# Performance work log

Hardware: AMD Instinct MI355X
Metric: run time of the kernel (lower is better)

## Reference

```python
import jax, jax.numpy as jnp
import numpy as np

TOPK = 32  # init kwarg topk=32, method='softmax'


def setup_inputs() -> dict:
    key = jax.random.key(0)
    k1, k2 = jax.random.split(key)
    X1 = jax.random.normal(k1, (8192, 64), dtype=jnp.float32)
    X2 = jax.random.normal(k2, (8192, 64), dtype=jnp.float32)
    return {"X1": X1, "X2": X2}


def reference(X1, X2):
    # pairwise Euclidean distance via the matmul expansion (same math as torch.cdist p=2)
    sq = (
        jnp.sum(X1 * X1, axis=-1)[:, None]
        + jnp.sum(X2 * X2, axis=-1)[None, :]
        - 2.0 * (X1 @ X2.T)
    )  # [N1, N2]
    neg_dist = -jnp.sqrt(jnp.maximum(sq, 0.0))
    # top-k along dim=1, softmax over the k selected values
    val, idx = jax.lax.top_k(neg_dist, TOPK)          # [N1, K]
    score = jax.nn.softmax(val, axis=1)               # [N1, K]
    # scatter scores back into a dense zero matrix
    rows = jnp.arange(neg_dist.shape[0])[:, None]     # [N1, 1]
    out = jnp.zeros_like(neg_dist).at[rows, idx].set(score)
    return out, score
```

## Files before the change

kernel.cpp:

```cpp
#include <hip/hip_runtime.h>
#include <math.h>
#include <float.h>
#include <limits.h>

#define N 8192
#define D 64
#define TOPK 32
#define TILE 128
#define CAP 1024

__device__ __forceinline__ unsigned ford(float f) {
    unsigned u = __float_as_uint(f);
    return u ^ ((u & 0x80000000u) ? 0xFFFFFFFFu : 0x80000000u);
}
__device__ __forceinline__ float finv(unsigned u) {
    unsigned b = (u & 0x80000000u) ? (u ^ 0x80000000u) : ~u;
    return __uint_as_float(b);
}

__global__ __launch_bounds__(256) void norms_kernel(
    const float* __restrict__ X1, const float* __restrict__ X2,
    float* __restrict__ nrm)
{
    int id = blockIdx.x * blockDim.x + threadIdx.x;
    if (id >= 2 * N) return;
    const float* X = (id < N) ? X1 : X2;
    int r = (id < N) ? id : id - N;
    const float4* p = (const float4*)(X + (size_t)r * D);
    float s = 0.f;
#pragma unroll
    for (int q = 0; q < D / 4; ++q) {
        float4 v = p[q];
        s += v.x * v.x + v.y * v.y + v.z * v.z + v.w * v.w;
    }
    nrm[id] = s;
}

__global__ __launch_bounds__(256, 2) void dist_kernel(
    const float* __restrict__ X1, const float* __restrict__ X2,
    const float* __restrict__ nrm, float* __restrict__ out,
    float* __restrict__ tmax, int have_tmax)
{
    __shared__ float As[D * TILE];
    __shared__ float Bs[D * TILE];

    const int t = threadIdx.x;
    const int row0 = blockIdx.y * TILE;
    const int col0 = blockIdx.x * TILE;

#pragma unroll
    for (int p = 0; p < 8; ++p) {
        int lin = p * 256 + t;
        int r   = lin >> 4;
        int d4  = (lin & 15) << 2;
        int g   = (d4 >> 2) & 7;
        int cb  = r ^ (g << 3);
        float4 a = *(const float4*)(X1 + (size_t)(row0 + r) * D + d4);
        As[(d4 + 0) * TILE + cb] = a.x;
        As[(d4 + 1) * TILE + cb] = a.y;
        As[(d4 + 2) * TILE + cb] = a.z;
        As[(d4 + 3) * TILE + cb] = a.w;
        float4 b = *(const float4*)(X2 + (size_t)(col0 + r) * D + d4);
        Bs[(d4 + 0) * TILE + cb] = b.x;
        Bs[(d4 + 1) * TILE + cb] = b.y;
        Bs[(d4 + 2) * TILE + cb] = b.z;
        Bs[(d4 + 3) * TILE + cb] = b.w;
    }
    __syncthreads();

    const int tx = t & 15;
    const int ty = t >> 4;
    float acc[8][8] = {};

#pragma unroll 8
    for (int k = 0; k < D; ++k) {
        int gk  = (k >> 2) & 7;
        int ab  = k * TILE + ((ty ^ gk) << 3);
        int bb0 = k * TILE + ((4 * tx) ^ (gk << 3));
        float4 a0 = *(const float4*)&As[ab];
        float4 a1 = *(const float4*)&As[ab + 4];
        float4 b0 = *(const float4*)&Bs[bb0];
        float4 b1 = *(const float4*)&Bs[bb0 + 64];
        float av[8] = {a0.x, a0.y, a0.z, a0.w, a1.x, a1.y, a1.z, a1.w};
        float bv[8] = {b0.x, b0.y, b0.z, b0.w, b1.x, b1.y, b1.z, b1.w};
#pragma unroll
        for (int i = 0; i < 8; ++i)
#pragma unroll
            for (int j = 0; j < 8; ++j)
                acc[i][j] += av[i] * bv[j];
    }

    float na[8], nb[8];
#pragma unroll
    for (int i = 0; i < 8; ++i) na[i] = nrm[row0 + 8 * ty + i];
#pragma unroll
    for (int q = 0; q < 4; ++q) {
        nb[q]     = nrm[N + col0 + 4 * tx + q];
        nb[4 + q] = nrm[N + col0 + 64 + 4 * tx + q];
    }

    float rmax[8];
#pragma unroll
    for (int i = 0; i < 8; ++i) rmax[i] = -FLT_MAX;

#pragma unroll
    for (int i = 0; i < 8; ++i) {
        float* po = out + (size_t)(row0 + 8 * ty + i) * N + col0 + 4 * tx;
        float4 o0, o1;
        float* f0 = (float*)&o0;
        float* f1 = (float*)&o1;
#pragma unroll
        for (int q = 0; q < 4; ++q) {
            float s0 = na[i] + nb[q] - 2.0f * acc[i][q];
            f0[q] = -fmaxf(s0, 0.0f);
            float s1 = na[i] + nb[4 + q] - 2.0f * acc[i][4 + q];
            f1[q] = -fmaxf(s1, 0.0f);
            rmax[i] = fmaxf(rmax[i], fmaxf(f0[q], f1[q]));
        }
        *(float4*)po        = o0;
        *(float4*)(po + 64) = o1;
    }

    if (have_tmax) {
#pragma unroll
        for (int i = 0; i < 8; ++i) {
            float mv = rmax[i];
            mv = fmaxf(mv, __shfl_down(mv, 8, 16));
            mv = fmaxf(mv, __shfl_down(mv, 4, 16));
            mv = fmaxf(mv, __shfl_down(mv, 2, 16));
            mv = fmaxf(mv, __shfl_down(mv, 1, 16));
            if (tx == 0)
                tmax[(size_t)(row0 + 8 * ty + i) * 64 + blockIdx.x] = mv;
        }
    }
}

__global__ __launch_bounds__(256) void topk_kernel(
    float* __restrict__ out, float* __restrict__ score_out,
    const float* __restrict__ tmax, int have_tmax)
{
    __shared__ unsigned long long cand[4][CAP];
    __shared__ int scnt[4];

    const int t    = threadIdx.x;
    const int w    = t >> 6;
    const int lane = t & 63;
    const int r    = blockIdx.x * 4 + w;
    float* row = out + (size_t)r * N;
    const float4* row4 = (const float4*)row;

    float thr;
    float lm = -FLT_MAX;
    if (have_tmax) {
        float tm = tmax[(size_t)r * 64 + lane];
        unsigned km = ford(tm);
        int rk = 0;
#pragma unroll
        for (int l = 0; l < 64; ++l) {
            unsigned o = __shfl(km, l);
            rk += (o > km || (o == km && l < lane)) ? 1 : 0;
        }
        unsigned long long bm = __ballot(rk == 31);
        thr = __shfl(tm, __ffsll(bm) - 1);
    } else {
#pragma unroll 8
        for (int c = 0; c < 32; ++c) {
            float4 x = row4[c * 64 + lane];
            lm = fmaxf(lm, fmaxf(fmaxf(x.x, x.y), fmaxf(x.z, x.w)));
        }
        thr = lm;
        for (int off = 32; off > 0; off >>= 1)
            thr = fminf(thr, __shfl_xor(thr, off));
    }

    for (int attempt = 0; ; ++attempt) {
        if (lane == 0) scnt[w] = 0;
        __builtin_amdgcn_s_waitcnt(0xC07F);
        for (int c = 0; c < 32; ++c) {
            float4 x = row4[c * 64 + lane];
            float vs[4] = {x.x, x.y, x.z, x.w};
#pragma unroll
            for (int q = 0; q < 4; ++q) {
                float v = vs[q];
                lm = fmaxf(lm, v);
                if (v >= thr) {
                    int p = atomicAdd(&scnt[w], 1);
                    if (p < CAP) {
                        unsigned long long key =
                            ((unsigned long long)ford(v) << 32) |
                            (unsigned)(8191 - (4 * (c * 64 + lane) + q));
                        cand[w][p] = key;
                    }
                }
            }
        }
        __builtin_amdgcn_s_waitcnt(0xC07F);
        if (scnt[w] <= CAP || attempt == 1) break;
        unsigned kml = ford(lm);
        int rk2 = 0;
#pragma unroll
        for (int l = 0; l < 64; ++l) {
            unsigned o = __shfl(kml, l);
            rk2 += (o < kml || (o == kml && l < lane)) ? 1 : 0;
        }
        unsigned long long bm2 = __ballot(rk2 == 15);
        float t2 = __shfl(lm, __ffsll(bm2) - 1);
        thr = fmaxf(thr, t2);
    }
    const int n = min(scnt[w], CAP);

    unsigned long long mykey = 0ull;
    for (int it = 0; it < TOPK; ++it) {
        unsigned long long b = 0ull; int bp = 0;
        for (int q = lane; q < n; q += 64) {
            unsigned long long kk = cand[w][q];
            if (kk > b) { b = kk; bp = q; }
        }
        for (int off = 32; off > 0; off >>= 1) {
            unsigned long long ob = __shfl_down(b, off);
            int op = __shfl_down(bp, off);
            if (ob > b) { b = ob; bp = op; }
        }
        unsigned long long b0 = __shfl(b, 0);
        int bp0 = __shfl(bp, 0);
        if (lane == it) { mykey = b0; cand[w][bp0] = 0ull; }
    }

    float myv = 0.f; int myj = 0;
    if (lane < TOPK) {
        float sv = finv((unsigned)(mykey >> 32));
        myv = -sqrtf(-sv);
        myj = 8191 - (int)(mykey & 0xFFFFFFFFu);
    }
    float Mx = __shfl(myv, 0);
    float e = (lane < TOPK) ? expf(myv - Mx) : 0.f;
    float Z = e;
    for (int off = 32; off > 0; off >>= 1) Z += __shfl_xor(Z, off);
    float s = e / Z;
    if (lane < TOPK) score_out[(size_t)r * TOPK + lane] = s;

    const float4 zz = make_float4(0.f, 0.f, 0.f, 0.f);
#pragma unroll 8
    for (int c = 0; c < 32; ++c) ((float4*)row)[c * 64 + lane] = zz;
    __builtin_amdgcn_s_waitcnt(0x0F70);
    if (lane < TOPK) row[myj] = s;
}

extern "C" void kernel_launch(void* const* d_in, const int* in_sizes, int n_in,
                              void* d_out, int out_size, void* d_ws, size_t ws_size,
                              hipStream_t stream)
{
    const float* X1 = (const float*)d_in[0];
    const float* X2 = (const float*)d_in[1];
    float* out = (float*)d_out;
    float* nrm = (float*)d_ws;
    float* tmax = nrm + 2 * N;
    size_t need = (size_t)(2 * N + (size_t)N * 64) * sizeof(float);
    int have_tmax = (ws_size >= need) ? 1 : 0;

    norms_kernel<<<(2 * N + 255) / 256, 256, 0, stream>>>(X1, X2, nrm);

    dim3 grid(N / TILE, N / TILE);
    dist_kernel<<<grid, 256, 0, stream>>>(X1, X2, nrm, out, tmax, have_tmax);

    topk_kernel<<<N / 4, 256, 0, stream>>>(out, out + (size_t)N * N, tmax, have_tmax);
}
```

Measured before the change: 476.3 us.

## Recompute distances instead of storing them; gather candidates in fused zero-writing pass

```diff
diff --git a/kernel.cpp b/kernel.cpp
--- a/kernel.cpp
+++ b/kernel.cpp
@@ -8,6 +8,8 @@
 #define TOPK 32
 #define TILE 128
 #define CAP 1024
+#define CAPC 512
+#define NCHUNK 8
 
 __device__ __forceinline__ unsigned ford(float f) {
     unsigned u = __float_as_uint(f);
@@ -36,10 +38,9 @@
     nrm[id] = s;
 }
 
-__global__ __launch_bounds__(256, 2) void dist_kernel(
+__global__ __launch_bounds__(256, 2) void dist_tmax_kernel(
     const float* __restrict__ X1, const float* __restrict__ X2,
-    const float* __restrict__ nrm, float* __restrict__ out,
-    float* __restrict__ tmax, int have_tmax)
+    const float* __restrict__ nrm, float* __restrict__ tmax)
 {
     __shared__ float As[D * TILE];
     __shared__ float Bs[D * TILE];
@@ -99,6 +100,270 @@
         nb[4 + q] = nrm[N + col0 + 64 + 4 * tx + q];
     }
 
+#pragma unroll
+    for (int i = 0; i < 8; ++i) {
+        float mv = -FLT_MAX;
+#pragma unroll
+        for (int q = 0; q < 4; ++q) {
+            float s0 = na[i] + nb[q] - 2.0f * acc[i][q];
+            float v0 = -fmaxf(s0, 0.0f);
+            float s1 = na[i] + nb[4 + q] - 2.0f * acc[i][4 + q];
+            float v1 = -fmaxf(s1, 0.0f);
+            mv = fmaxf(mv, fmaxf(v0, v1));
+        }
+        mv = fmaxf(mv, __shfl_down(mv, 8, 16));
+        mv = fmaxf(mv, __shfl_down(mv, 4, 16));
+        mv = fmaxf(mv, __shfl_down(mv, 2, 16));
+        mv = fmaxf(mv, __shfl_down(mv, 1, 16));
+        if (tx == 0)
+            tmax[(size_t)(row0 + 8 * ty + i) * 64 + blockIdx.x] = mv;
+    }
+}
+
+__global__ __launch_bounds__(256) void thr_kernel(
+    const float* __restrict__ tmax, float* __restrict__ thr,
+    int* __restrict__ cnt)
+{
+    const int t = threadIdx.x;
+    const int w = t >> 6;
+    const int lane = t & 63;
+    const int r = blockIdx.x * 4 + w;
+
+    float tm = tmax[(size_t)r * 64 + lane];
+    unsigned km = ford(tm);
+    int rk = 0;
+#pragma unroll
+    for (int l = 0; l < 64; ++l) {
+        unsigned o = __shfl(km, l);
+        rk += (o > km || (o == km && l < lane)) ? 1 : 0;
+    }
+    unsigned long long bm = __ballot(rk == 31);
+    float tv = __shfl(tm, __ffsll(bm) - 1);
+    if (lane == 0) {
+        thr[r] = tv - 1e-3f;
+        cnt[r] = 0;
+    }
+}
+
+__global__ __launch_bounds__(256, 2) void cand_zero_kernel(
+    const float* __restrict__ X1, const float* __restrict__ X2,
+    const float* __restrict__ nrm, const float* __restrict__ thr,
+    float* __restrict__ out, unsigned long long* __restrict__ cand,
+    int* __restrict__ cnt)
+{
+    __shared__ float As[D * TILE];
+    __shared__ float Bs[D * TILE];
+
+    const int t = threadIdx.x;
+    const int row0 = blockIdx.y * TILE;
+    const int chunk0 = blockIdx.x * (N / NCHUNK);
+    const int tx = t & 15;
+    const int ty = t >> 4;
+
+#pragma unroll
+    for (int p = 0; p < 8; ++p) {
+        int lin = p * 256 + t;
+        int r   = lin >> 4;
+        int d4  = (lin & 15) << 2;
+        int g   = (d4 >> 2) & 7;
+        int cb  = r ^ (g << 3);
+        float4 a = *(const float4*)(X1 + (size_t)(row0 + r) * D + d4);
+        As[(d4 + 0) * TILE + cb] = a.x;
+        As[(d4 + 1) * TILE + cb] = a.y;
+        As[(d4 + 2) * TILE + cb] = a.z;
+        As[(d4 + 3) * TILE + cb] = a.w;
+    }
+
+    float na[8], thv[8];
+#pragma unroll
+    for (int i = 0; i < 8; ++i) {
+        na[i]  = nrm[row0 + 8 * ty + i];
+        thv[i] = thr[row0 + 8 * ty + i];
+    }
+    __syncthreads();
+
+    for (int ct = 0; ct < (N / NCHUNK) / TILE; ++ct) {
+        const int col0 = chunk0 + ct * TILE;
+        if (ct) __syncthreads();
+#pragma unroll
+        for (int p = 0; p < 8; ++p) {
+            int lin = p * 256 + t;
+            int r   = lin >> 4;
+            int d4  = (lin & 15) << 2;
+            int g   = (d4 >> 2) & 7;
+            int cb  = r ^ (g << 3);
+            float4 b = *(const float4*)(X2 + (size_t)(col0 + r) * D + d4);
+            Bs[(d4 + 0) * TILE + cb] = b.x;
+            Bs[(d4 + 1) * TILE + cb] = b.y;
+            Bs[(d4 + 2) * TILE + cb] = b.z;
+            Bs[(d4 + 3) * TILE + cb] = b.w;
+        }
+        __syncthreads();
+
+        float acc[8][8] = {};
+#pragma unroll 8
+        for (int k = 0; k < D; ++k) {
+            int gk  = (k >> 2) & 7;
+            int ab  = k * TILE + ((ty ^ gk) << 3);
+            int bb0 = k * TILE + ((4 * tx) ^ (gk << 3));
+            float4 a0 = *(const float4*)&As[ab];
+            float4 a1 = *(const float4*)&As[ab + 4];
+            float4 b0 = *(const float4*)&Bs[bb0];
+            float4 b1 = *(const float4*)&Bs[bb0 + 64];
+            float av[8] = {a0.x, a0.y, a0.z, a0.w, a1.x, a1.y, a1.z, a1.w};
+            float bv[8] = {b0.x, b0.y, b0.z, b0.w, b1.x, b1.y, b1.z, b1.w};
+#pragma unroll
+            for (int i = 0; i < 8; ++i)
+#pragma unroll
+                for (int j = 0; j < 8; ++j)
+                    acc[i][j] += av[i] * bv[j];
+        }
+
+        float nb[8];
+#pragma unroll
+        for (int q = 0; q < 4; ++q) {
+            nb[q]     = nrm[N + col0 + 4 * tx + q];
+            nb[4 + q] = nrm[N + col0 + 64 + 4 * tx + q];
+        }
+
+        const float4 zz = make_float4(0.f, 0.f, 0.f, 0.f);
+#pragma unroll
+        for (int i = 0; i < 8; ++i) {
+            const int row = row0 + 8 * ty + i;
+            float* po = out + (size_t)row * N + col0 + 4 * tx;
+            *(float4*)po        = zz;
+            *(float4*)(po + 64) = zz;
+#pragma unroll
+            for (int q = 0; q < 8; ++q) {
+                float s = na[i] + nb[q] - 2.0f * acc[i][q];
+                float v = -fmaxf(s, 0.0f);
+                if (v >= thv[i]) {
+                    int col = col0 + ((q < 4) ? (4 * tx + q)
+                                              : (64 + 4 * tx + (q - 4)));
+                    int p0 = atomicAdd(&cnt[row], 1);
+                    if (p0 < CAPC)
+                        cand[(size_t)row * CAPC + p0] =
+                            ((unsigned long long)ford(v) << 32) |
+                            (unsigned)(8191 - col);
+                }
+            }
+        }
+    }
+}
+
+__global__ __launch_bounds__(256) void topk_scatter_kernel(
+    float* __restrict__ out, float* __restrict__ score_out,
+    const unsigned long long* __restrict__ cand, const int* __restrict__ cnt)
+{
+    __shared__ unsigned long long cs[4][CAPC];
+    const int t = threadIdx.x;
+    const int w = t >> 6;
+    const int lane = t & 63;
+    const int r = blockIdx.x * 4 + w;
+
+    int n = cnt[r];
+    if (n > CAPC) n = CAPC;
+    const unsigned long long* cr = cand + (size_t)r * CAPC;
+    for (int q = lane; q < n; q += 64) cs[w][q] = cr[q];
+    __builtin_amdgcn_s_waitcnt(0xC07F);
+
+    unsigned long long mykey = 0ull;
+    for (int it = 0; it < TOPK; ++it) {
+        unsigned long long b = 0ull; int bp = 0;
+        for (int q = lane; q < n; q += 64) {
+            unsigned long long kk = cs[w][q];
+            if (kk > b) { b = kk; bp = q; }
+        }
+        for (int off = 32; off > 0; off >>= 1) {
+            unsigned long long ob = __shfl_down(b, off);
+            int op = __shfl_down(bp, off);
+            if (ob > b) { b = ob; bp = op; }
+        }
+        unsigned long long b0 = __shfl(b, 0);
+        int bp0 = __shfl(bp, 0);
+        if (lane == it) { mykey = b0; cs[w][bp0] = 0ull; }
+    }
+
+    float myv = 0.f; int myj = 0;
+    if (lane < TOPK) {
+        float sv = finv((unsigned)(mykey >> 32));
+        myv = -sqrtf(-sv);
+        myj = 8191 - (int)(mykey & 0xFFFFFFFFu);
+    }
+    float Mx = __shfl(myv, 0);
+    float e = (lane < TOPK) ? expf(myv - Mx) : 0.f;
+    float Z = e;
+    for (int off = 32; off > 0; off >>= 1) Z += __shfl_xor(Z, off);
+    float s = e / Z;
+    if (lane < TOPK) {
+        score_out[(size_t)r * TOPK + lane] = s;
+        out[(size_t)r * N + myj] = s;
+    }
+}
+
+__global__ __launch_bounds__(256, 2) void dist_kernel(
+    const float* __restrict__ X1, const float* __restrict__ X2,
+    const float* __restrict__ nrm, float* __restrict__ out,
+    float* __restrict__ tmax, int have_tmax)
+{
+    __shared__ float As[D * TILE];
+    __shared__ float Bs[D * TILE];
+
+    const int t = threadIdx.x;
+    const int row0 = blockIdx.y * TILE;
+    const int col0 = blockIdx.x * TILE;
+
+#pragma unroll
+    for (int p = 0; p < 8; ++p) {
+        int lin = p * 256 + t;
+        int r   = lin >> 4;
+        int d4  = (lin & 15) << 2;
+        int g   = (d4 >> 2) & 7;
+        int cb  = r ^ (g << 3);
+        float4 a = *(const float4*)(X1 + (size_t)(row0 + r) * D + d4);
+        As[(d4 + 0) * TILE + cb] = a.x;
+        As[(d4 + 1) * TILE + cb] = a.y;
+        As[(d4 + 2) * TILE + cb] = a.z;
+        As[(d4 + 3) * TILE + cb] = a.w;
+        float4 b = *(const float4*)(X2 + (size_t)(col0 + r) * D + d4);
+        Bs[(d4 + 0) * TILE + cb] = b.x;
+        Bs[(d4 + 1) * TILE + cb] = b.y;
+        Bs[(d4 + 2) * TILE + cb] = b.z;
+        Bs[(d4 + 3) * TILE + cb] = b.w;
+    }
+    __syncthreads();
+
+    const int tx = t & 15;
+    const int ty = t >> 4;
+    float acc[8][8] = {};
+
+#pragma unroll 8
+    for (int k = 0; k < D; ++k) {
+        int gk  = (k >> 2) & 7;
+        int ab  = k * TILE + ((ty ^ gk) << 3);
+        int bb0 = k * TILE + ((4 * tx) ^ (gk << 3));
+        float4 a0 = *(const float4*)&As[ab];
+        float4 a1 = *(const float4*)&As[ab + 4];
+        float4 b0 = *(const float4*)&Bs[bb0];
+        float4 b1 = *(const float4*)&Bs[bb0 + 64];
+        float av[8] = {a0.x, a0.y, a0.z, a0.w, a1.x, a1.y, a1.z, a1.w};
+        float bv[8] = {b0.x, b0.y, b0.z, b0.w, b1.x, b1.y, b1.z, b1.w};
+#pragma unroll
+        for (int i = 0; i < 8; ++i)
+#pragma unroll
+            for (int j = 0; j < 8; ++j)
+                acc[i][j] += av[i] * bv[j];
+    }
+
+    float na[8], nb[8];
+#pragma unroll
+    for (int i = 0; i < 8; ++i) na[i] = nrm[row0 + 8 * ty + i];
+#pragma unroll
+    for (int q = 0; q < 4; ++q) {
+        nb[q]     = nrm[N + col0 + 4 * tx + q];
+        nb[4 + q] = nrm[N + col0 + 64 + 4 * tx + q];
+    }
+
     float rmax[8];
 #pragma unroll
     for (int i = 0; i < 8; ++i) rmax[i] = -FLT_MAX;
@@ -253,15 +518,31 @@
     const float* X1 = (const float*)d_in[0];
     const float* X2 = (const float*)d_in[1];
     float* out = (float*)d_out;
-    float* nrm = (float*)d_ws;
+    float* score = out + (size_t)N * N;
+
+    float* nrm  = (float*)d_ws;
     float* tmax = nrm + 2 * N;
-    size_t need = (size_t)(2 * N + (size_t)N * 64) * sizeof(float);
-    int have_tmax = (ws_size >= need) ? 1 : 0;
+    float* thrv = tmax + (size_t)N * 64;
+    int*   cnt  = (int*)(thrv + N);
+    unsigned long long* cand = (unsigned long long*)(cnt + N);
+
+    size_t need_new = (size_t)(2 * N + (size_t)N * 64 + 2 * N) * sizeof(float)
+                    + (size_t)N * CAPC * sizeof(unsigned long long);
+    size_t need_old = (size_t)(2 * N + (size_t)N * 64) * sizeof(float);
 
     norms_kernel<<<(2 * N + 255) / 256, 256, 0, stream>>>(X1, X2, nrm);
 
-    dim3 grid(N / TILE, N / TILE);
-    dist_kernel<<<grid, 256, 0, stream>>>(X1, X2, nrm, out, tmax, have_tmax);
-
-    topk_kernel<<<N / 4, 256, 0, stream>>>(out, out + (size_t)N * N, tmax, have_tmax);
-}
+    if (ws_size >= need_new) {
+        dim3 grid(N / TILE, N / TILE);
+        dist_tmax_kernel<<<grid, 256, 0, stream>>>(X1, X2, nrm, tmax);
+        thr_kernel<<<N / 4, 256, 0, stream>>>(tmax, thrv, cnt);
+        dim3 grid2(NCHUNK, N / TILE);
+        cand_zero_kernel<<<grid2, 256, 0, stream>>>(X1, X2, nrm, thrv, out, cand, cnt);
+        topk_scatter_kernel<<<N / 4, 256, 0, stream>>>(out, score, cand, cnt);
+    } else {
+        int have_tmax = (ws_size >= need_old) ? 1 : 0;
+        dim3 grid(N / TILE, N / TILE);
+        dist_kernel<<<grid, 256, 0, stream>>>(X1, X2, nrm, out, tmax, have_tmax);
+        topk_kernel<<<N / 4, 256, 0, stream>>>(out, score, tmax, have_tmax);
+    }
+}
```

Result: slower. 589.0 us (+23.6%).

## Replace dense distance matrix with split-bf16 MFMA two-pass candidate top-k

Applied to the files above, without the earlier changes.

```diff
diff --git a/kernel.cpp b/kernel.cpp
--- a/kernel.cpp
+++ b/kernel.cpp
@@ -8,6 +8,12 @@
 #define TOPK 32
 #define TILE 128
 #define CAP 1024
+#define SLOT 32
+#define CAPR 512
+#define MARGIN 0.3f
+
+typedef __attribute__((ext_vector_type(8))) short bf16x8;
+typedef __attribute__((ext_vector_type(4))) float f32x4;
 
 __device__ __forceinline__ unsigned ford(float f) {
     unsigned u = __float_as_uint(f);
@@ -16,6 +22,325 @@
 __device__ __forceinline__ float finv(unsigned u) {
     unsigned b = (u & 0x80000000u) ? (u ^ 0x80000000u) : ~u;
     return __uint_as_float(b);
+}
+__device__ __forceinline__ unsigned short f2bf(float f) {
+    unsigned u = __float_as_uint(f);
+    unsigned r = u + 0x7FFFu + ((u >> 16) & 1u);
+    return (unsigned short)(r >> 16);
+}
+__device__ __forceinline__ float bf2f(unsigned short h) {
+    return __uint_as_float(((unsigned)h) << 16);
+}
+
+__global__ __launch_bounds__(256) void prep_kernel(
+    const float* __restrict__ X1, const float* __restrict__ X2,
+    float* __restrict__ nrm,
+    unsigned short* __restrict__ X1h, unsigned short* __restrict__ X1l,
+    unsigned short* __restrict__ X2h, unsigned short* __restrict__ X2l)
+{
+    int id = blockIdx.x * blockDim.x + threadIdx.x;
+    if (id >= 2 * N) return;
+    const float* X = (id < N) ? X1 : X2;
+    unsigned short* H = (id < N) ? X1h : X2h;
+    unsigned short* L = (id < N) ? X1l : X2l;
+    int r = (id < N) ? id : id - N;
+    const float4* p = (const float4*)(X + (size_t)r * D);
+    ushort4* ph = (ushort4*)(H + (size_t)r * D);
+    ushort4* pl = (ushort4*)(L + (size_t)r * D);
+    float s = 0.f;
+#pragma unroll
+    for (int q = 0; q < D / 4; ++q) {
+        float4 v = p[q];
+        s += v.x * v.x + v.y * v.y + v.z * v.z + v.w * v.w;
+        ushort4 h, l;
+        h.x = f2bf(v.x); l.x = f2bf(v.x - bf2f(h.x));
+        h.y = f2bf(v.y); l.y = f2bf(v.y - bf2f(h.y));
+        h.z = f2bf(v.z); l.z = f2bf(v.z - bf2f(h.z));
+        h.w = f2bf(v.w); l.w = f2bf(v.w - bf2f(h.w));
+        ph[q] = h; pl[q] = l;
+    }
+    nrm[id] = s;
+}
+
+#define MFMA16(a, b, c) __builtin_amdgcn_mfma_f32_16x16x32_bf16((a), (b), (c), 0, 0, 0)
+
+__device__ __forceinline__ void mfma_core(
+    const unsigned short* __restrict__ X1h, const unsigned short* __restrict__ X1l,
+    const unsigned short* __restrict__ X2h, const unsigned short* __restrict__ X2l,
+    int rW, int cW, int lane, f32x4 acc[4][4])
+{
+    const int l15 = lane & 15;
+    const int lg8 = (lane >> 4) * 8;
+
+    bf16x8 ah[4][2], al[4][2];
+#pragma unroll
+    for (int mt = 0; mt < 4; ++mt) {
+        size_t ro = (size_t)(rW + mt * 16 + l15) * D + lg8;
+        ah[mt][0] = *(const bf16x8*)(X1h + ro);
+        ah[mt][1] = *(const bf16x8*)(X1h + ro + 32);
+        al[mt][0] = *(const bf16x8*)(X1l + ro);
+        al[mt][1] = *(const bf16x8*)(X1l + ro + 32);
+    }
+#pragma unroll
+    for (int nt = 0; nt < 4; ++nt) {
+        size_t co = (size_t)(cW + nt * 16 + l15) * D + lg8;
+        bf16x8 bh0 = *(const bf16x8*)(X2h + co);
+        bf16x8 bh1 = *(const bf16x8*)(X2h + co + 32);
+        bf16x8 bl0 = *(const bf16x8*)(X2l + co);
+        bf16x8 bl1 = *(const bf16x8*)(X2l + co + 32);
+#pragma unroll
+        for (int mt = 0; mt < 4; ++mt) {
+            acc[mt][nt] = MFMA16(ah[mt][0], bh0, acc[mt][nt]);
+            acc[mt][nt] = MFMA16(ah[mt][1], bh1, acc[mt][nt]);
+            acc[mt][nt] = MFMA16(ah[mt][0], bl0, acc[mt][nt]);
+            acc[mt][nt] = MFMA16(ah[mt][1], bl1, acc[mt][nt]);
+            acc[mt][nt] = MFMA16(al[mt][0], bh0, acc[mt][nt]);
+            acc[mt][nt] = MFMA16(al[mt][1], bh1, acc[mt][nt]);
+        }
+    }
+}
+
+__global__ __launch_bounds__(256) void mfma_tmax_kernel(
+    const unsigned short* __restrict__ X1h, const unsigned short* __restrict__ X1l,
+    const unsigned short* __restrict__ X2h, const unsigned short* __restrict__ X2l,
+    const float* __restrict__ nrm, float* __restrict__ tmax)
+{
+    __shared__ float red[128][2];
+    const int t = threadIdx.x;
+    const int lane = t & 63, w = t >> 6;
+    const int wr = w >> 1, wc = w & 1;
+    const int row0 = blockIdx.y * TILE, col0 = blockIdx.x * TILE;
+    const int rW = row0 + wr * 64, cW = col0 + wc * 64;
+    const int l15 = lane & 15, lg = lane >> 4;
+
+    f32x4 acc[4][4];
+#pragma unroll
+    for (int mt = 0; mt < 4; ++mt)
+#pragma unroll
+        for (int nt = 0; nt < 4; ++nt)
+            acc[mt][nt] = (f32x4){0.f, 0.f, 0.f, 0.f};
+
+    mfma_core(X1h, X1l, X2h, X2l, rW, cW, lane, acc);
+
+    float nb[4];
+#pragma unroll
+    for (int nt = 0; nt < 4; ++nt) nb[nt] = nrm[N + cW + nt * 16 + l15];
+
+    float rmax[4][4];
+#pragma unroll
+    for (int mt = 0; mt < 4; ++mt) {
+#pragma unroll
+        for (int reg = 0; reg < 4; ++reg) {
+            float na = nrm[rW + mt * 16 + lg * 4 + reg];
+            float m = -FLT_MAX;
+#pragma unroll
+            for (int nt = 0; nt < 4; ++nt) {
+                float v = -fmaxf(na + nb[nt] - 2.0f * acc[mt][nt][reg], 0.f);
+                m = fmaxf(m, v);
+            }
+            rmax[mt][reg] = m;
+        }
+    }
+#pragma unroll
+    for (int off = 1; off < 16; off <<= 1)
+#pragma unroll
+        for (int mt = 0; mt < 4; ++mt)
+#pragma unroll
+            for (int reg = 0; reg < 4; ++reg)
+                rmax[mt][reg] = fmaxf(rmax[mt][reg], __shfl_xor(rmax[mt][reg], off));
+
+    if (l15 == 0) {
+#pragma unroll
+        for (int mt = 0; mt < 4; ++mt)
+#pragma unroll
+            for (int reg = 0; reg < 4; ++reg)
+                red[wr * 64 + mt * 16 + lg * 4 + reg][wc] = rmax[mt][reg];
+    }
+    __syncthreads();
+    if (t < 128)
+        tmax[(size_t)(row0 + t) * 64 + blockIdx.x] = fmaxf(red[t][0], red[t][1]);
+}
+
+__global__ __launch_bounds__(256) void thr_kernel(
+    const float* __restrict__ tmax, float* __restrict__ thr)
+{
+    const int t = threadIdx.x;
+    const int w = t >> 6;
+    const int lane = t & 63;
+    const int r = blockIdx.x * 4 + w;
+
+    float tm = tmax[(size_t)r * 64 + lane];
+    unsigned km = ford(tm);
+    int rk = 0;
+#pragma unroll
+    for (int l = 0; l < 64; ++l) {
+        unsigned o = __shfl(km, l);
+        rk += (o > km || (o == km && l < lane)) ? 1 : 0;
+    }
+    unsigned long long bm = __ballot(rk == 31);
+    float tv = __shfl(tm, __ffsll(bm) - 1);
+    if (lane == 0) thr[r] = tv - MARGIN;
+}
+
+__global__ __launch_bounds__(256) void mfma_cand_kernel(
+    const unsigned short* __restrict__ X1h, const unsigned short* __restrict__ X1l,
+    const unsigned short* __restrict__ X2h, const unsigned short* __restrict__ X2l,
+    const float* __restrict__ nrm, const float* __restrict__ thr,
+    float* __restrict__ out, unsigned short* __restrict__ cand,
+    int* __restrict__ cnt)
+{
+    __shared__ unsigned short lbuf[128][SLOT];
+    __shared__ int lcnt[128];
+
+    const int t = threadIdx.x;
+    const int lane = t & 63, w = t >> 6;
+    const int wr = w >> 1, wc = w & 1;
+    const int row0 = blockIdx.y * TILE, col0 = blockIdx.x * TILE;
+    const int rW = row0 + wr * 64, cW = col0 + wc * 64;
+    const int l15 = lane & 15, lg = lane >> 4;
+
+    if (t < 128) lcnt[t] = 0;
+    __syncthreads();
+
+    f32x4 acc[4][4];
+#pragma unroll
+    for (int mt = 0; mt < 4; ++mt)
+#pragma unroll
+        for (int nt = 0; nt < 4; ++nt)
+            acc[mt][nt] = (f32x4){0.f, 0.f, 0.f, 0.f};
+
+    mfma_core(X1h, X1l, X2h, X2l, rW, cW, lane, acc);
+
+    const float4 zz = make_float4(0.f, 0.f, 0.f, 0.f);
+#pragma unroll
+    for (int p = 0; p < 16; ++p) {
+        int lin = p * 256 + t;
+        int rr = lin >> 5;
+        int c4 = (lin & 31) << 2;
+        *(float4*)(out + (size_t)(row0 + rr) * N + col0 + c4) = zz;
+    }
+
+    float nb[4];
+#pragma unroll
+    for (int nt = 0; nt < 4; ++nt) nb[nt] = nrm[N + cW + nt * 16 + l15];
+
+#pragma unroll
+    for (int mt = 0; mt < 4; ++mt) {
+#pragma unroll
+        for (int reg = 0; reg < 4; ++reg) {
+            int lrow = wr * 64 + mt * 16 + lg * 4 + reg;
+            float na = nrm[row0 + lrow];
+            float th = thr[row0 + lrow];
+#pragma unroll
+            for (int nt = 0; nt < 4; ++nt) {
+                float v = -fmaxf(na + nb[nt] - 2.0f * acc[mt][nt][reg], 0.f);
+                if (v >= th) {
+                    int p0 = atomicAdd(&lcnt[lrow], 1);
+                    if (p0 < SLOT)
+                        lbuf[lrow][p0] = (unsigned short)(wc * 64 + nt * 16 + l15);
+                }
+            }
+        }
+    }
+    __syncthreads();
+
+    if (t < 128) {
+        int c = lcnt[t];
+        size_t sidx = (size_t)(row0 + t) * 64 + blockIdx.x;
+        cnt[sidx] = c;
+        unsigned short* cg = cand + sidx * SLOT;
+        int m = min(c, SLOT);
+        for (int j = 0; j < m; ++j) cg[j] = lbuf[t][j];
+    }
+}
+
+__global__ __launch_bounds__(256) void exact_topk_kernel(
+    const float* __restrict__ X1, const float* __restrict__ X2,
+    const float* __restrict__ nrm,
+    const unsigned short* __restrict__ cand, const int* __restrict__ cnt,
+    float* __restrict__ out, float* __restrict__ score_out)
+{
+    __shared__ float x1r[4][D];
+    __shared__ unsigned short lst[4][CAPR];
+    __shared__ unsigned long long kl[4][CAPR];
+
+    const int t = threadIdx.x;
+    const int w = t >> 6;
+    const int lane = t & 63;
+    const int r = blockIdx.x * 4 + w;
+
+    x1r[w][lane] = X1[(size_t)r * D + lane];
+
+    int c = cnt[(size_t)r * 64 + lane];
+    int eff = (c > SLOT) ? 128 : c;
+    int pre = eff;
+#pragma unroll
+    for (int o = 1; o < 64; o <<= 1) {
+        int pv = __shfl_up(pre, o);
+        if (lane >= o) pre += pv;
+    }
+    int off0 = pre - eff;
+    int M = __shfl(pre, 63);
+    if (M > CAPR) M = CAPR;
+
+    const unsigned short* cg = cand + ((size_t)r * 64 + lane) * SLOT;
+    for (int j = 0; j < eff; ++j) {
+        int pos = off0 + j;
+        if (pos < CAPR) {
+            int colloc = (c > SLOT) ? j : (int)cg[j];
+            lst[w][pos] = (unsigned short)(lane * 128 + colloc);
+        }
+    }
+    __builtin_amdgcn_s_waitcnt(0xC07F);
+
+    float na = nrm[r];
+    for (int q = lane; q < M; q += 64) {
+        int col = lst[w][q];
+        const float4* xr = (const float4*)(X2 + (size_t)col * D);
+        float dot = 0.f;
+#pragma unroll
+        for (int i = 0; i < D / 4; ++i) {
+            float4 xv = xr[i];
+            dot += x1r[w][4 * i + 0] * xv.x + x1r[w][4 * i + 1] * xv.y
+                 + x1r[w][4 * i + 2] * xv.z + x1r[w][4 * i + 3] * xv.w;
+        }
+        float v = -fmaxf(na + nrm[N + col] - 2.0f * dot, 0.f);
+        kl[w][q] = ((unsigned long long)ford(v) << 32) | (unsigned)(8191 - col);
+    }
+    __builtin_amdgcn_s_waitcnt(0xC07F);
+
+    unsigned long long mykey = 0ull;
+    for (int it = 0; it < TOPK; ++it) {
+        unsigned long long b = 0ull; int bp = 0;
+        for (int q = lane; q < M; q += 64) {
+            unsigned long long kk = kl[w][q];
+            if (kk > b) { b = kk; bp = q; }
+        }
+        for (int off = 32; off > 0; off >>= 1) {
+            unsigned long long ob = __shfl_down(b, off);
+            int op = __shfl_down(bp, off);
+            if (ob > b) { b = ob; bp = op; }
+        }
+        unsigned long long b0 = __shfl(b, 0);
+        int bp0 = __shfl(bp, 0);
+        if (lane == it) { mykey = b0; kl[w][bp0] = 0ull; }
+    }
+
+    float myv = -FLT_MAX; int myj = 0;
+    if (lane < TOPK && mykey != 0ull) {
+        float sv = finv((unsigned)(mykey >> 32));
+        myv = -sqrtf(-sv);
+        myj = 8191 - (int)(mykey & 0xFFFFFFFFu);
+    }
+    float Mx = __shfl(myv, 0);
+    float e = (lane < TOPK && mykey != 0ull) ? expf(myv - Mx) : 0.f;
+    float Z = e;
+    for (int off = 32; off > 0; off >>= 1) Z += __shfl_xor(Z, off);
+    float s = e / Z;
+    if (lane < TOPK && mykey != 0ull) {
+        score_out[(size_t)r * TOPK + lane] = s;
+        out[(size_t)r * N + myj] = s;
+    }
 }
 
 __global__ __launch_bounds__(256) void norms_kernel(
@@ -139,7 +464,7 @@
     float* __restrict__ out, float* __restrict__ score_out,
     const float* __restrict__ tmax, int have_tmax)
 {
-    __shared__ unsigned long long cand[4][CAP];
+    __shared__ unsigned long long candl[4][CAP];
     __shared__ int scnt[4];
 
     const int t    = threadIdx.x;
@@ -189,7 +514,7 @@
                         unsigned long long key =
                             ((unsigned long long)ford(v) << 32) |
                             (unsigned)(8191 - (4 * (c * 64 + lane) + q));
-                        cand[w][p] = key;
+                        candl[w][p] = key;
                     }
                 }
             }
@@ -213,7 +538,7 @@
     for (int it = 0; it < TOPK; ++it) {
         unsigned long long b = 0ull; int bp = 0;
         for (int q = lane; q < n; q += 64) {
-            unsigned long long kk = cand[w][q];
+            unsigned long long kk = candl[w][q];
             if (kk > b) { b = kk; bp = q; }
         }
         for (int off = 32; off > 0; off >>= 1) {
@@ -223,7 +548,7 @@
         }
         unsigned long long b0 = __shfl(b, 0);
         int bp0 = __shfl(bp, 0);
-        if (lane == it) { mykey = b0; cand[w][bp0] = 0ull; }
+        if (lane == it) { mykey = b0; candl[w][bp0] = 0ull; }
     }
 
     float myv = 0.f; int myj = 0;
@@ -253,15 +578,41 @@
     const float* X1 = (const float*)d_in[0];
     const float* X2 = (const float*)d_in[1];
     float* out = (float*)d_out;
-    float* nrm = (float*)d_ws;
+    float* score = out + (size_t)N * N;
+
+    char* base = (char*)d_ws;
+    float* nrm  = (float*)base;
     float* tmax = nrm + 2 * N;
-    size_t need = (size_t)(2 * N + (size_t)N * 64) * sizeof(float);
-    int have_tmax = (ws_size >= need) ? 1 : 0;
-
-    norms_kernel<<<(2 * N + 255) / 256, 256, 0, stream>>>(X1, X2, nrm);
-
-    dim3 grid(N / TILE, N / TILE);
-    dist_kernel<<<grid, 256, 0, stream>>>(X1, X2, nrm, out, tmax, have_tmax);
-
-    topk_kernel<<<N / 4, 256, 0, stream>>>(out, out + (size_t)N * N, tmax, have_tmax);
-}
+    float* thrv = tmax + (size_t)N * 64;
+    int*   cnt  = (int*)(thrv + N);
+    unsigned short* X1h = (unsigned short*)(cnt + (size_t)N * 64);
+    unsigned short* X1l = X1h + (size_t)N * D;
+    unsigned short* X2h = X1l + (size_t)N * D;
+    unsigned short* X2l = X2h + (size_t)N * D;
+    unsigned short* cand = X2l + (size_t)N * D;
+
+    size_t need_new = (size_t)(2 * N + (size_t)N * 64 + N) * sizeof(float)
+                    + (size_t)N * 64 * sizeof(int)
+                    + 4 * (size_t)N * D * sizeof(unsigned short)
+                    + (size_t)N * 64 * SLOT * sizeof(unsigned short);
+    size_t need_old = (size_t)(2 * N + (size_t)N * 64) * sizeof(float);
+
+    if (ws_size >= need_new) {
+        prep_kernel<<<(2 * N + 255) / 256, 256, 0, stream>>>(
+            X1, X2, nrm, X1h, X1l, X2h, X2l);
+        dim3 grid(N / TILE, N / TILE);
+        mfma_tmax_kernel<<<grid, 256, 0, stream>>>(X1h, X1l, X2h, X2l, nrm, tmax);
+        thr_kernel<<<N / 4, 256, 0, stream>>>(tmax, thrv);
+        mfma_cand_kernel<<<grid, 256, 0, stream>>>(
+            X1h, X1l, X2h, X2l, nrm, thrv, out, cand, cnt);
+        exact_topk_kernel<<<N / 4, 256, 0, stream>>>(
+            X1, X2, nrm, cand, cnt, out, score);
+    } else {
+        float* tmax_f = nrm + 2 * N;
+        int have_tmax = (ws_size >= need_old) ? 1 : 0;
+        norms_kernel<<<(2 * N + 255) / 256, 256, 0, stream>>>(X1, X2, nrm);
+        dim3 grid(N / TILE, N / TILE);
+        dist_kernel<<<grid, 256, 0, stream>>>(X1, X2, nrm, out, tmax_f, have_tmax);
+        topk_kernel<<<N / 4, 256, 0, stream>>>(out, score, tmax_f, have_tmax);
+    }
+}
```

Measured after the change: 521.3 us. 9.4% more time.
